# Optimization experiments

Hardware: AMD Instinct MI355X
Metric: run time of the kernel (lower is better)

The kernel has to match this reference:

```python
import jax, jax.numpy as jnp
import numpy as np

CHANNEL = 256
REDUCTION = 4
GAMMA = 0.5
H_BW = 1.0  # kernel bandwidth h


def setup_inputs() -> dict:
    key = jax.random.key(0)
    k_x, k1, k2, k3, k4 = jax.random.split(key, 5)
    c, r = CHANNEL, CHANNEL // REDUCTION
    x = jax.random.normal(k_x, (32, c, 64, 64), dtype=jnp.float32)
    # fc params, stored as [in, out] for y = x @ W + b (matches nn.Linear math)
    w1 = jax.random.normal(k1, (c, r), dtype=jnp.float32) * (1.0 / np.sqrt(c))
    b1 = jax.random.normal(k2, (r,), dtype=jnp.float32) * 0.01
    w2 = jax.random.normal(k3, (r, c), dtype=jnp.float32) * (1.0 / np.sqrt(r))
    b2 = jax.random.normal(k4, (c,), dtype=jnp.float32) * 0.01
    return {"x": x, "w1": w1, "b1": b1, "w2": w2, "b2": b2}


def reference(x, w1, b1, w2, b2):
    b, c, Hh, Ww = x.shape
    xf = x.reshape(b, c, Hh * Ww)                      # [b, c, n]
    sq = jnp.sum(xf * xf, axis=-1)                     # [b, c]
    gram = jnp.einsum('bcn,bdn->bcd', xf, xf)          # [b, c, c]
    # ||x_i - x_j||^2 = |x_i|^2 + |x_j|^2 - 2 x_i.x_j  (clamped for numerics)
    d2 = jnp.maximum(sq[:, :, None] + sq[:, None, :] - 2.0 * gram, 0.0)
    K = jnp.exp(-0.5 * d2 / (H_BW * H_BW))             # gaussian kernel on dist
    density = jnp.sum(K, axis=-1) / c                  # [b, c]
    hid = jax.nn.relu(density @ w1 + b1)               # [b, c//r]
    attn = jax.nn.sigmoid(hid @ w2 + b2)               # [b, c]
    return x * (attn[:, :, None, None] + GAMMA)
```

## Files before the change

### kernel.cpp

```cpp
#include <hip/hip_runtime.h>
#include <hip/hip_bf16.h>
#include <cstdint>
#include <cstddef>

#define BATCH 32
#define CH    256
#define NSP   4096
#define RED   64
#define GAMMA 0.5f
#define NSPLIT 4
#define KSEG  (NSP / NSPLIT)
#define NKT   (KSEG / 64)
#define TILE_ELEMS (128 * 128)
#define SLICE_STRIDE ((size_t)BATCH * 4 * TILE_ELEMS)

typedef float f32x4 __attribute__((ext_vector_type(4)));
typedef short short8 __attribute__((ext_vector_type(8)));

static __device__ inline unsigned short bfu(float f) {
  __hip_bfloat16 h = __float2bfloat16(f);
  return __builtin_bit_cast(unsigned short, h);
}
static __device__ inline float bf2f(unsigned short u) {
  return __uint_as_float(((uint32_t)u) << 16);
}

__global__ __launch_bounds__(512, 4)
void gram_partial_kernel(const float* __restrict__ x,
                         unsigned short* __restrict__ gpart) {
  const int bx   = blockIdx.x;
  const int xcd  = bx & 7;
  const int slot = bx >> 3;
  const int b    = xcd * 4 + (slot >> 4);
  const int rem  = slot & 15;
  const int tile = rem >> 2;
  const int s    = rem & 3;
  const int tr   = tile >> 1;
  const int tc   = tile & 1;
  const bool diag = (tr == tc);
  const int tid  = threadIdx.x;
  const int lane = tid & 63;
  const int wave = tid >> 6;
  const int wr   = wave >> 2;
  const int wc   = wave & 3;

  __shared__ unsigned short lA[128 * 64];
  __shared__ unsigned short lB[128 * 64];

  const int rsub = tid >> 4;
  const int c4   = tid & 15;

  const float* baseA = x + (size_t)(b * CH + tr * 128) * NSP + s * KSEG;
  const float* baseB = x + (size_t)(b * CH + tc * 128) * NSP + s * KSEG;

  f32x4 pa[4], pb[4];
#pragma unroll
  for (int i = 0; i < 4; ++i) {
    int row = i * 32 + rsub;
    pa[i] = *reinterpret_cast<const f32x4*>(baseA + (size_t)row * NSP + c4 * 4);
  }
  if (!diag) {
#pragma unroll
    for (int i = 0; i < 4; ++i) {
      int row = i * 32 + rsub;
      pb[i] = *reinterpret_cast<const f32x4*>(baseB + (size_t)row * NSP + c4 * 4);
    }
  }

  f32x4 acc[4][2];
#pragma unroll
  for (int m = 0; m < 4; ++m)
#pragma unroll
    for (int n = 0; n < 2; ++n)
      acc[m][n] = (f32x4){0.f, 0.f, 0.f, 0.f};

  char* cA = (char*)lA;
  char* cB = diag ? cA : (char*)lB;

  for (int kt = 0; kt < NKT; ++kt) {
    __syncthreads();
#pragma unroll
    for (int i = 0; i < 4; ++i) {
      int row = i * 32 + rsub;
      int byte = row * 128 + c4 * 8;
      byte ^= (row & 7) << 4;

      uint64_t wa = (uint64_t)bfu(pa[i][0]) | ((uint64_t)bfu(pa[i][1]) << 16) |
                    ((uint64_t)bfu(pa[i][2]) << 32) | ((uint64_t)bfu(pa[i][3]) << 48);
      *reinterpret_cast<uint64_t*>(cA + byte) = wa;

      if (!diag) {
        uint64_t wb = (uint64_t)bfu(pb[i][0]) | ((uint64_t)bfu(pb[i][1]) << 16) |
                      ((uint64_t)bfu(pb[i][2]) << 32) | ((uint64_t)bfu(pb[i][3]) << 48);
        *reinterpret_cast<uint64_t*>(cB + byte) = wb;
      }
    }
    __syncthreads();

    if (kt + 1 < NKT) {
      const float* kA = baseA + (kt + 1) * 64;
#pragma unroll
      for (int i = 0; i < 4; ++i) {
        int row = i * 32 + rsub;
        pa[i] = *reinterpret_cast<const f32x4*>(kA + (size_t)row * NSP + c4 * 4);
      }
      if (!diag) {
        const float* kB = baseB + (kt + 1) * 64;
#pragma unroll
        for (int i = 0; i < 4; ++i) {
          int row = i * 32 + rsub;
          pb[i] = *reinterpret_cast<const f32x4*>(kB + (size_t)row * NSP + c4 * 4);
        }
      }
    }

    short8 af[4][2], bff[2][2];
#pragma unroll
    for (int m = 0; m < 4; ++m)
#pragma unroll
      for (int kh = 0; kh < 2; ++kh) {
        int rowa = wr * 64 + m * 16 + (lane & 15);
        int bytea = rowa * 128 + kh * 64 + ((lane >> 4) * 16);
        bytea ^= (rowa & 7) << 4;
        af[m][kh] = *reinterpret_cast<const short8*>(cA + bytea);
      }
#pragma unroll
    for (int n = 0; n < 2; ++n)
#pragma unroll
      for (int kh = 0; kh < 2; ++kh) {
        int rowb = wc * 32 + n * 16 + (lane & 15);
        int byteb = rowb * 128 + kh * 64 + ((lane >> 4) * 16);
        byteb ^= (rowb & 7) << 4;
        bff[n][kh] = *reinterpret_cast<const short8*>(cB + byteb);
      }

#pragma unroll
    for (int m = 0; m < 4; ++m)
#pragma unroll
      for (int n = 0; n < 2; ++n)
#pragma unroll
        for (int kh = 0; kh < 2; ++kh)
          acc[m][n] = __builtin_amdgcn_mfma_f32_16x16x32_bf16(
              af[m][kh], bff[n][kh], acc[m][n], 0, 0, 0);
  }

  unsigned short* g = gpart + ((size_t)s * BATCH + b) * 4 * TILE_ELEMS
                            + (size_t)tile * TILE_ELEMS;
#pragma unroll
  for (int m = 0; m < 4; ++m)
#pragma unroll
    for (int n = 0; n < 2; ++n)
#pragma unroll
      for (int r = 0; r < 4; ++r) {
        int row = wr * 64 + m * 16 + ((lane >> 4) * 4 + r);
        int col = wc * 32 + n * 16 + (lane & 15);
        g[row * 128 + col] = bfu(acc[m][n][r]);
      }
}

__global__ __launch_bounds__(256)
void density_kernel(const unsigned short* __restrict__ gpart,
                    float* __restrict__ density) {
  const int blk  = blockIdx.x;
  const int b    = blk >> 3;
  const int rg   = blk & 7;
  const int t    = threadIdx.x;
  const int lane = t & 63;
  const int wave = t >> 6;

  __shared__ float sq[CH];
  {
    int jt = t >> 7, jr = t & 127;
    size_t off = ((size_t)b * 4 + (size_t)jt * 3) * TILE_ELEMS + (size_t)jr * 129;
    float v = 0.f;
#pragma unroll
    for (int s = 0; s < NSPLIT; ++s) v += bf2f(gpart[off + (size_t)s * SLICE_STRIDE]);
    sq[t] = v;
  }
  __syncthreads();

  const unsigned short* gb = gpart + (size_t)b * 4 * TILE_ELEMS;
#pragma unroll 1
  for (int rr = 0; rr < 8; ++rr) {
    int r = rg * 32 + wave * 8 + rr;
    int rt = r >> 7, rrow = r & 127;
    float sqr = sq[r];
    float ssum = 0.f;
#pragma unroll
    for (int cc = 0; cc < 4; ++cc) {
      int j = cc * 64 + lane;
      int jt = j >> 7;
      size_t off = (size_t)(rt * 2 + jt) * TILE_ELEMS + (size_t)rrow * 128 + (j & 127);
      float g = 0.f;
#pragma unroll
      for (int s = 0; s < NSPLIT; ++s) g += bf2f(gb[off + (size_t)s * SLICE_STRIDE]);
      float d2 = fmaxf(sqr + sq[j] - 2.f * g, 0.f);
      ssum += __expf(-0.5f * d2);
    }
    ssum += __shfl_xor(ssum, 1);
    ssum += __shfl_xor(ssum, 2);
    ssum += __shfl_xor(ssum, 4);
    ssum += __shfl_xor(ssum, 8);
    ssum += __shfl_xor(ssum, 16);
    ssum += __shfl_xor(ssum, 32);
    if (lane == 0) density[b * CH + r] = ssum * (1.0f / CH);
  }
}

__global__ __launch_bounds__(256)
void mlp_kernel(const float* __restrict__ density,
                const float* __restrict__ w1, const float* __restrict__ b1,
                const float* __restrict__ w2, const float* __restrict__ b2,
                float* __restrict__ scale) {
  const int b = blockIdx.x;
  const int t = threadIdx.x;
  __shared__ float dens[CH];
  __shared__ float hid[RED];
  dens[t] = density[b * CH + t];
  __syncthreads();
  if (t < RED) {
    float s = b1[t];
#pragma unroll 4
    for (int c = 0; c < CH; ++c) s += dens[c] * w1[c * RED + t];
    hid[t] = fmaxf(s, 0.f);
  }
  __syncthreads();
  float s = b2[t];
#pragma unroll
  for (int h = 0; h < RED; ++h) s += hid[h] * w2[h * CH + t];
  scale[b * CH + t] = 1.f / (1.f + __expf(-s)) + GAMMA;
}

__global__ __launch_bounds__(256)
void scale_kernel(const f32x4* __restrict__ x, const float* __restrict__ scale,
                  f32x4* __restrict__ out, int n4) {
  const int stride = gridDim.x * blockDim.x;
  for (int i = blockIdx.x * blockDim.x + threadIdx.x; i < n4; i += stride) {
    float s = scale[i >> 10];
    __builtin_nontemporal_store(x[i] * s, &out[i]);
  }
}

extern "C" void kernel_launch(void* const* d_in, const int* in_sizes, int n_in,
                              void* d_out, int out_size, void* d_ws, size_t ws_size,
                              hipStream_t stream) {
  const float* x  = (const float*)d_in[0];
  const float* w1 = (const float*)d_in[1];
  const float* b1 = (const float*)d_in[2];
  const float* w2 = (const float*)d_in[3];
  const float* b2 = (const float*)d_in[4];
  float* out = (float*)d_out;

  unsigned short* gpart = (unsigned short*)d_ws;
  float* density = (float*)(gpart + NSPLIT * SLICE_STRIDE);
  float* scale   = density + BATCH * CH;

  gram_partial_kernel<<<dim3(BATCH * 4 * NSPLIT), dim3(512), 0, stream>>>(x, gpart);
  density_kernel<<<dim3(BATCH * 8), dim3(256), 0, stream>>>(gpart, density);
  mlp_kernel<<<dim3(BATCH), dim3(256), 0, stream>>>(density, w1, b1, w2, b2, scale);

  const int n4 = BATCH * CH * NSP / 4;
  scale_kernel<<<dim3(4096), dim3(256), 0, stream>>>(
      (const f32x4*)x, scale, (f32x4*)out, n4);
}
```

Before: 111.1 us.

## Split gram K dimension eight ways, drop diagonal LDS sharing, vectorize density loads

Doubles the K-split of the gram partial kernel from 4 to 8 slices, doubling the grid, and raises the launch-bounds occupancy hint to 8 blocks. It also removes the diagonal-tile special case, so every block loads and converts both A and B tiles. Finally, the density kernel reads bf16 partial gram values in pairs as 32-bit loads. The aim is more parallelism and better latency hiding in the gram stage, paid for by twice as many bf16 partials to write and reduce and by redundant B loads on diagonal tiles.

```diff
diff --git a/kernel.cpp b/kernel.cpp
--- a/kernel.cpp
+++ b/kernel.cpp
@@ -8,7 +8,7 @@
 #define NSP   4096
 #define RED   64
 #define GAMMA 0.5f
-#define NSPLIT 4
+#define NSPLIT 8
 #define KSEG  (NSP / NSPLIT)
 #define NKT   (KSEG / 64)
 #define TILE_ELEMS (128 * 128)
@@ -25,19 +25,18 @@
   return __uint_as_float(((uint32_t)u) << 16);
 }
 
-__global__ __launch_bounds__(512, 4)
+__global__ __launch_bounds__(512, 8)
 void gram_partial_kernel(const float* __restrict__ x,
                          unsigned short* __restrict__ gpart) {
   const int bx   = blockIdx.x;
   const int xcd  = bx & 7;
   const int slot = bx >> 3;
-  const int b    = xcd * 4 + (slot >> 4);
-  const int rem  = slot & 15;
-  const int tile = rem >> 2;
-  const int s    = rem & 3;
+  const int b    = xcd * 4 + (slot >> 5);
+  const int rem  = slot & 31;
+  const int tile = rem >> 3;
+  const int s    = rem & 7;
   const int tr   = tile >> 1;
   const int tc   = tile & 1;
-  const bool diag = (tr == tc);
   const int tid  = threadIdx.x;
   const int lane = tid & 63;
   const int wave = tid >> 6;
@@ -58,13 +57,7 @@
   for (int i = 0; i < 4; ++i) {
     int row = i * 32 + rsub;
     pa[i] = *reinterpret_cast<const f32x4*>(baseA + (size_t)row * NSP + c4 * 4);
-  }
-  if (!diag) {
-#pragma unroll
-    for (int i = 0; i < 4; ++i) {
-      int row = i * 32 + rsub;
-      pb[i] = *reinterpret_cast<const f32x4*>(baseB + (size_t)row * NSP + c4 * 4);
-    }
+    pb[i] = *reinterpret_cast<const f32x4*>(baseB + (size_t)row * NSP + c4 * 4);
   }
 
   f32x4 acc[4][2];
@@ -75,7 +68,7 @@
       acc[m][n] = (f32x4){0.f, 0.f, 0.f, 0.f};
 
   char* cA = (char*)lA;
-  char* cB = diag ? cA : (char*)lB;
+  char* cB = (char*)lB;
 
   for (int kt = 0; kt < NKT; ++kt) {
     __syncthreads();
@@ -89,28 +82,20 @@
                     ((uint64_t)bfu(pa[i][2]) << 32) | ((uint64_t)bfu(pa[i][3]) << 48);
       *reinterpret_cast<uint64_t*>(cA + byte) = wa;
 
-      if (!diag) {
-        uint64_t wb = (uint64_t)bfu(pb[i][0]) | ((uint64_t)bfu(pb[i][1]) << 16) |
-                      ((uint64_t)bfu(pb[i][2]) << 32) | ((uint64_t)bfu(pb[i][3]) << 48);
-        *reinterpret_cast<uint64_t*>(cB + byte) = wb;
-      }
+      uint64_t wb = (uint64_t)bfu(pb[i][0]) | ((uint64_t)bfu(pb[i][1]) << 16) |
+                    ((uint64_t)bfu(pb[i][2]) << 32) | ((uint64_t)bfu(pb[i][3]) << 48);
+      *reinterpret_cast<uint64_t*>(cB + byte) = wb;
     }
     __syncthreads();
 
     if (kt + 1 < NKT) {
       const float* kA = baseA + (kt + 1) * 64;
+      const float* kB = baseB + (kt + 1) * 64;
 #pragma unroll
       for (int i = 0; i < 4; ++i) {
         int row = i * 32 + rsub;
         pa[i] = *reinterpret_cast<const f32x4*>(kA + (size_t)row * NSP + c4 * 4);
-      }
-      if (!diag) {
-        const float* kB = baseB + (kt + 1) * 64;
-#pragma unroll
-        for (int i = 0; i < 4; ++i) {
-          int row = i * 32 + rsub;
-          pb[i] = *reinterpret_cast<const f32x4*>(kB + (size_t)row * NSP + c4 * 4);
-        }
+        pb[i] = *reinterpret_cast<const f32x4*>(kB + (size_t)row * NSP + c4 * 4);
       }
     }
 
@@ -187,15 +172,19 @@
     float sqr = sq[r];
     float ssum = 0.f;
 #pragma unroll
-    for (int cc = 0; cc < 4; ++cc) {
-      int j = cc * 64 + lane;
-      int jt = j >> 7;
-      size_t off = (size_t)(rt * 2 + jt) * TILE_ELEMS + (size_t)rrow * 128 + (j & 127);
-      float g = 0.f;
-#pragma unroll
-      for (int s = 0; s < NSPLIT; ++s) g += bf2f(gb[off + (size_t)s * SLICE_STRIDE]);
-      float d2 = fmaxf(sqr + sq[j] - 2.f * g, 0.f);
-      ssum += __expf(-0.5f * d2);
+    for (int cc = 0; cc < 2; ++cc) {
+      int j0 = cc * 128 + lane * 2;
+      size_t off = (size_t)(rt * 2 + cc) * TILE_ELEMS + (size_t)rrow * 128 + (j0 & 127);
+      float g0 = 0.f, g1 = 0.f;
+#pragma unroll
+      for (int s = 0; s < NSPLIT; ++s) {
+        uint32_t pair = *reinterpret_cast<const uint32_t*>(gb + off + (size_t)s * SLICE_STRIDE);
+        g0 += __uint_as_float((pair & 0xffffu) << 16);
+        g1 += __uint_as_float(pair & 0xffff0000u);
+      }
+      float d20 = fmaxf(sqr + sq[j0]     - 2.f * g0, 0.f);
+      float d21 = fmaxf(sqr + sq[j0 + 1] - 2.f * g1, 0.f);
+      ssum += __expf(-0.5f * d20) + __expf(-0.5f * d21);
     }
     ssum += __shfl_xor(ssum, 1);
     ssum += __shfl_xor(ssum, 2);
```

Measured after the change: 183.4 us. 65.1% more time.
